# Kernel optimization log

Measured on AMD Instinct MI355X. Metric: run time of the kernel, lower is better.

## Reference

```python
import jax, jax.numpy as jnp
import numpy as np

TOKENS = 8192
IN_F = 4096
OUT_F = 4096
QMAX = 127.0  # int8 symmetric quant range
EPS = 1e-8


def setup_inputs() -> dict:
    key = jax.random.key(0)
    k1, k2, k3, k4 = jax.random.split(key, 4)
    x = jax.random.normal(k1, (TOKENS, IN_F), dtype=jnp.float32)
    # Pre-quantized int8 weight [out_features, in_features]
    weight_q = jax.random.randint(k2, (OUT_F, IN_F), -127, 128, dtype=jnp.int8)
    # Per-output-channel weight scales (realistic small magnitudes)
    weight_scale = jax.random.uniform(k3, (OUT_F,), dtype=jnp.float32) * 0.01 + 1e-3
    bias = jax.random.normal(k4, (OUT_F,), dtype=jnp.float32)
    return {"x": x, "weight_q": weight_q, "weight_scale": weight_scale, "bias": bias}


def reference(x, weight_q, weight_scale, bias):
    # Dynamic per-token symmetric int8 activation quantization
    absmax = jnp.max(jnp.abs(x), axis=-1, keepdims=True)           # [T, 1]
    x_scale = jnp.maximum(absmax, EPS) / QMAX                      # [T, 1]
    x_q = jnp.clip(jnp.round(x / x_scale), -QMAX, QMAX).astype(jnp.int8)
    acc = jax.lax.dot_general(
        x_q, weight_q,
        dimension_numbers=(((1,), (1,)), ((), ())),
        preferred_element_type=jnp.int32,
    )
    # Inline dequant: per-token activation scale * per-channel weight scale
    out = acc.astype(jnp.float32) * x_scale * weight_scale[None, :]
    out = out + bias[None, :]
    return out
```

## Files before the change

### kernel.cpp

```cpp
#include <hip/hip_runtime.h>
#include <cstdint>
#include <cstddef>

#define TOKENS 8192
#define IN_F   4096
#define OUT_F  4096
#define QMAXF  127.0f
#define EPSF   1e-8f

typedef int   int32x4 __attribute__((ext_vector_type(4)));

__device__ __forceinline__ void gload16(const void* g, void* l) {
    __builtin_amdgcn_global_load_lds(
        (const __attribute__((address_space(1))) void*)g,
        (__attribute__((address_space(3))) void*)l,
        16, 0, 0);
}

__device__ __forceinline__ int quant1(float v, float inv) {
    int q = (int)rintf(v * inv);
    q = q > 127 ? 127 : q;
    q = q < -127 ? -127 : q;
    return q;
}

__device__ __forceinline__ unsigned int pack4i(int a, int b, int c, int d) {
    return (unsigned int)(a & 255) | ((unsigned int)(b & 255) << 8) |
           ((unsigned int)(c & 255) << 16) | ((unsigned int)(d & 255) << 24);
}

__global__ __launch_bounds__(256) void quant_x_kernel(const float* __restrict__ x,
                                                      signed char* __restrict__ xq,
                                                      float* __restrict__ xscale) {
    const int t   = blockIdx.x;
    const int tid = threadIdx.x;
    const float* xr = x + (size_t)t * IN_F + tid * 16;

    float4 v[4];
    float am = 0.0f;
#pragma unroll
    for (int i = 0; i < 4; ++i) {
        v[i] = ((const float4*)xr)[i];
        am = fmaxf(am, fmaxf(fmaxf(fabsf(v[i].x), fabsf(v[i].y)),
                             fmaxf(fabsf(v[i].z), fabsf(v[i].w))));
    }
#pragma unroll
    for (int off = 32; off >= 1; off >>= 1)
        am = fmaxf(am, __shfl_xor(am, off));

    __shared__ float wmax[4];
    const int wid = tid >> 6, lane = tid & 63;
    if (lane == 0) wmax[wid] = am;
    __syncthreads();
    am = fmaxf(fmaxf(wmax[0], wmax[1]), fmaxf(wmax[2], wmax[3]));

    const float s   = fmaxf(am, EPSF) / QMAXF;
    const float inv = QMAXF / fmaxf(am, EPSF);
    if (tid == 0) xscale[t] = s;

    unsigned int w[4];
#pragma unroll
    for (int i = 0; i < 4; ++i) {
        w[i] = pack4i(quant1(v[i].x, inv), quant1(v[i].y, inv),
                      quant1(v[i].z, inv), quant1(v[i].w, inv));
    }
    *(uint4*)(xq + (size_t)t * IN_F + tid * 16) = make_uint4(w[0], w[1], w[2], w[3]);
}

__global__ __launch_bounds__(256) void pack_w_kernel(const int* __restrict__ w,
                                                     signed char* __restrict__ wq) {
    const size_t idx = (size_t)blockIdx.x * 256 + threadIdx.x;
    const int4* src = (const int4*)w + idx * 4;
    unsigned int o[4];
#pragma unroll
    for (int i = 0; i < 4; ++i) {
        int4 u = src[i];
        o[i] = pack4i(u.x, u.y, u.z, u.w);
    }
    ((uint4*)wq)[idx] = make_uint4(o[0], o[1], o[2], o[3]);
}

__global__ __launch_bounds__(256) void gemm_kernel(const signed char* __restrict__ xq,
                                                   const signed char* __restrict__ wq,
                                                   const float* __restrict__ xscale,
                                                   const float* __restrict__ wscale,
                                                   const float* __restrict__ bias,
                                                   float* __restrict__ out) {
    __shared__ __align__(16) signed char As[128 * 64];
    __shared__ __align__(16) signed char Bs[128 * 64];

    const int tid  = threadIdx.x;
    const int wid  = tid >> 6;
    const int lane = tid & 63;
    const int bid  = blockIdx.x;
    const int bn0  = (bid & 31) * 128;
    const int bm0  = (bid >> 5) * 128;

    const int rt = tid >> 2;
    const int ct = (tid & 3) * 16;
    const signed char* pa0 = xq + (size_t)(bm0 + rt) * IN_F + ct;
    const signed char* pa1 = xq + (size_t)(bm0 + 64 + rt) * IN_F + ct;
    const signed char* pb0 = wq + (size_t)(bn0 + rt) * IN_F + ct;
    const signed char* pb1 = wq + (size_t)(bn0 + 64 + rt) * IN_F + ct;
    signed char* lA0 = As + wid * 1024;
    signed char* lA1 = As + 4096 + wid * 1024;
    signed char* lB0 = Bs + wid * 1024;
    signed char* lB1 = Bs + 4096 + wid * 1024;

    const int wr = wid >> 1, wc = wid & 1;
    const int rA = wr * 64 + (lane & 15);
    const int rB = wc * 64 + (lane & 15);
    const int kb = (lane >> 4) * 16;

    int32x4 acc[4][4] = {};

    for (int kt = 0; kt < IN_F; kt += 64) {
        gload16(pa0 + kt, lA0);
        gload16(pa1 + kt, lA1);
        gload16(pb0 + kt, lB0);
        gload16(pb1 + kt, lB1);
        __syncthreads();

        int32x4 a[4], b[4];
#pragma unroll
        for (int m = 0; m < 4; ++m)
            a[m] = *(const int32x4*)&As[(rA + m * 16) * 64 + kb];
#pragma unroll
        for (int n = 0; n < 4; ++n)
            b[n] = *(const int32x4*)&Bs[(rB + n * 16) * 64 + kb];
#pragma unroll
        for (int m = 0; m < 4; ++m)
#pragma unroll
            for (int n = 0; n < 4; ++n)
                acc[m][n] = __builtin_amdgcn_mfma_i32_16x16x64_i8(a[m], b[n], acc[m][n], 0, 0, 0);
        __syncthreads();
    }

    const int r0 = bm0 + wr * 64 + (lane >> 4) * 4;
    const int c0 = bn0 + wc * 64 + (lane & 15);
#pragma unroll
    for (int n = 0; n < 4; ++n) {
        const int col = c0 + n * 16;
        const float wsc = wscale[col];
        const float bv  = bias[col];
#pragma unroll
        for (int m = 0; m < 4; ++m) {
#pragma unroll
            for (int j = 0; j < 4; ++j) {
                const int row = r0 + m * 16 + j;
                out[(size_t)row * OUT_F + col] =
                    (float)acc[m][n][j] * xscale[row] * wsc + bv;
            }
        }
    }
}

extern "C" void kernel_launch(void* const* d_in, const int* in_sizes, int n_in,
                              void* d_out, int out_size, void* d_ws, size_t ws_size,
                              hipStream_t stream) {
    const float* x      = (const float*)d_in[0];
    const int*   w      = (const int*)d_in[1];
    const float* wscale = (const float*)d_in[2];
    const float* bias   = (const float*)d_in[3];
    float* out = (float*)d_out;

    char* ws = (char*)d_ws;
    signed char* xq  = (signed char*)ws;
    signed char* wq8 = (signed char*)(ws + (size_t)TOKENS * IN_F);
    float* xscale    = (float*)(ws + (size_t)TOKENS * IN_F + (size_t)OUT_F * IN_F);

    quant_x_kernel<<<TOKENS, 256, 0, stream>>>(x, xq, xscale);
    pack_w_kernel<<<(OUT_F * (IN_F / 16)) / 256, 256, 0, stream>>>(w, wq8);
    gemm_kernel<<<(TOKENS / 128) * (OUT_F / 128), 256, 0, stream>>>(
        xq, wq8, xscale, wscale, bias, out);
}
```

Baseline: 235.0 us.

## Rewrite int8 GEMM with 256x256 tiles, triple-buffered LDS pipeline and 32x32 MFMA

```diff
diff --git a/kernel.cpp b/kernel.cpp
--- a/kernel.cpp
+++ b/kernel.cpp
@@ -8,13 +8,25 @@
 #define QMAXF  127.0f
 #define EPSF   1e-8f
 
-typedef int   int32x4 __attribute__((ext_vector_type(4)));
+typedef int i32x4  __attribute__((ext_vector_type(4)));
+typedef int i32x16 __attribute__((ext_vector_type(16)));
+
+#define BKB 64
+#define NT  (IN_F / BKB)
+#define LDS_BUF   32768
+#define LDS_TOTAL (3 * LDS_BUF)
 
 __device__ __forceinline__ void gload16(const void* g, void* l) {
     __builtin_amdgcn_global_load_lds(
         (const __attribute__((address_space(1))) void*)g,
         (__attribute__((address_space(3))) void*)l,
         16, 0, 0);
+}
+
+__device__ __forceinline__ void bar() {
+    asm volatile("" ::: "memory");
+    __builtin_amdgcn_s_barrier();
+    asm volatile("" ::: "memory");
 }
 
 __device__ __forceinline__ int quant1(float v, float inv) {
@@ -80,76 +92,143 @@
     ((uint4*)wq)[idx] = make_uint4(o[0], o[1], o[2], o[3]);
 }
 
-__global__ __launch_bounds__(256) void gemm_kernel(const signed char* __restrict__ xq,
-                                                   const signed char* __restrict__ wq,
-                                                   const float* __restrict__ xscale,
-                                                   const float* __restrict__ wscale,
-                                                   const float* __restrict__ bias,
-                                                   float* __restrict__ out) {
-    __shared__ __align__(16) signed char As[128 * 64];
-    __shared__ __align__(16) signed char Bs[128 * 64];
+__global__ __launch_bounds__(512, 2) void gemm_kernel(const signed char* __restrict__ xq,
+                                                      const signed char* __restrict__ wq,
+                                                      const float* __restrict__ xscale,
+                                                      const float* __restrict__ wscale,
+                                                      const float* __restrict__ bias,
+                                                      float* __restrict__ out) {
+    extern __shared__ __align__(16) char lds[];
 
     const int tid  = threadIdx.x;
     const int wid  = tid >> 6;
     const int lane = tid & 63;
+    const int wr   = wid >> 2;
+    const int wc   = wid & 3;
     const int bid  = blockIdx.x;
-    const int bn0  = (bid & 31) * 128;
-    const int bm0  = (bid >> 5) * 128;
-
-    const int rt = tid >> 2;
-    const int ct = (tid & 3) * 16;
-    const signed char* pa0 = xq + (size_t)(bm0 + rt) * IN_F + ct;
-    const signed char* pa1 = xq + (size_t)(bm0 + 64 + rt) * IN_F + ct;
-    const signed char* pb0 = wq + (size_t)(bn0 + rt) * IN_F + ct;
-    const signed char* pb1 = wq + (size_t)(bn0 + 64 + rt) * IN_F + ct;
-    signed char* lA0 = As + wid * 1024;
-    signed char* lA1 = As + 4096 + wid * 1024;
-    signed char* lB0 = Bs + wid * 1024;
-    signed char* lB1 = Bs + 4096 + wid * 1024;
-
-    const int wr = wid >> 1, wc = wid & 1;
-    const int rA = wr * 64 + (lane & 15);
-    const int rB = wc * 64 + (lane & 15);
-    const int kb = (lane >> 4) * 16;
-
-    int32x4 acc[4][4] = {};
-
-    for (int kt = 0; kt < IN_F; kt += 64) {
-        gload16(pa0 + kt, lA0);
-        gload16(pa1 + kt, lA1);
-        gload16(pb0 + kt, lB0);
-        gload16(pb1 + kt, lB1);
-        __syncthreads();
-
-        int32x4 a[4], b[4];
+    const int bm0  = (bid & 31) * 256;
+    const int bn0  = (bid >> 5) * 256;
+
+    const int srow = tid >> 2;
+    const int sg   = tid & 3;
+    const int scol = ((sg ^ (srow & 3)) << 4);
+    const signed char* gA0 = xq + (size_t)(bm0 + srow)       * IN_F + scol;
+    const signed char* gA1 = xq + (size_t)(bm0 + 128 + srow) * IN_F + scol;
+    const signed char* gB0 = wq + (size_t)(bn0 + srow)       * IN_F + scol;
+    const signed char* gB1 = wq + (size_t)(bn0 + 128 + srow) * IN_F + scol;
+    const int ldst = tid * 16;
+
+    const int l31 = lane & 31, hi = lane >> 5, l3 = lane & 3;
+    int a_off[4][2], b_off[2][2];
+#pragma unroll
+    for (int m = 0; m < 4; ++m) {
+        const int row = wr * 128 + m * 32 + l31;
+#pragma unroll
+        for (int ks = 0; ks < 2; ++ks)
+            a_off[m][ks] = row * 64 + (((ks * 2 + hi) ^ l3) << 4);
+    }
+#pragma unroll
+    for (int n = 0; n < 2; ++n) {
+        const int row = wc * 64 + n * 32 + l31;
+#pragma unroll
+        for (int ks = 0; ks < 2; ++ks)
+            b_off[n][ks] = 16384 + row * 64 + (((ks * 2 + hi) ^ l3) << 4);
+    }
+
+    i32x16 acc[4][2];
+#pragma unroll
+    for (int m = 0; m < 4; ++m)
+#pragma unroll
+        for (int n = 0; n < 2; ++n)
+#pragma unroll
+            for (int r = 0; r < 16; ++r) acc[m][n][r] = 0;
+
+    {
+        char* S0 = lds;
+        gload16(gA0,       S0 + ldst);
+        gload16(gA1,       S0 + 8192  + ldst);
+        gload16(gB0,       S0 + 16384 + ldst);
+        gload16(gB1,       S0 + 24576 + ldst);
+        char* S1 = lds + LDS_BUF;
+        gload16(gA0 + BKB, S1 + ldst);
+        gload16(gA1 + BKB, S1 + 8192  + ldst);
+        gload16(gB0 + BKB, S1 + 16384 + ldst);
+        gload16(gB1 + BKB, S1 + 24576 + ldst);
+    }
+    asm volatile("s_waitcnt vmcnt(4)" ::: "memory");
+    bar();
+
+    int cur = 0, nxt = 2;
+    for (int t = 0; t < NT; ++t) {
+        const char* Ab = lds + cur * LDS_BUF;
+        char* Sd = lds + nxt * LDS_BUF;
+        const bool st = (t + 2 < NT);
+        const int koff = (t + 2) * BKB;
+
+        i32x4 a0[4], b0[2];
+#pragma unroll
+        for (int m = 0; m < 4; ++m) a0[m] = *(const i32x4*)(Ab + a_off[m][0]);
+#pragma unroll
+        for (int n = 0; n < 2; ++n) b0[n] = *(const i32x4*)(Ab + b_off[n][0]);
+        if (st) {
+            gload16(gA0 + koff, Sd + ldst);
+            gload16(gB0 + koff, Sd + 16384 + ldst);
+        }
+        bar();
+        __builtin_amdgcn_s_setprio(1);
 #pragma unroll
         for (int m = 0; m < 4; ++m)
-            a[m] = *(const int32x4*)&As[(rA + m * 16) * 64 + kb];
-#pragma unroll
-        for (int n = 0; n < 4; ++n)
-            b[n] = *(const int32x4*)&Bs[(rB + n * 16) * 64 + kb];
+#pragma unroll
+            for (int n = 0; n < 2; ++n)
+                acc[m][n] = __builtin_amdgcn_mfma_i32_32x32x32_i8(a0[m], b0[n], acc[m][n], 0, 0, 0);
+        __builtin_amdgcn_s_setprio(0);
+        bar();
+
+        i32x4 a1[4], b1[2];
+#pragma unroll
+        for (int m = 0; m < 4; ++m) a1[m] = *(const i32x4*)(Ab + a_off[m][1]);
+#pragma unroll
+        for (int n = 0; n < 2; ++n) b1[n] = *(const i32x4*)(Ab + b_off[n][1]);
+        if (st) {
+            gload16(gA1 + koff, Sd + 8192  + ldst);
+            gload16(gB1 + koff, Sd + 24576 + ldst);
+        }
+        bar();
+        __builtin_amdgcn_s_setprio(1);
 #pragma unroll
         for (int m = 0; m < 4; ++m)
 #pragma unroll
-            for (int n = 0; n < 4; ++n)
-                acc[m][n] = __builtin_amdgcn_mfma_i32_16x16x64_i8(a[m], b[n], acc[m][n], 0, 0, 0);
-        __syncthreads();
-    }
-
-    const int r0 = bm0 + wr * 64 + (lane >> 4) * 4;
-    const int c0 = bn0 + wc * 64 + (lane & 15);
-#pragma unroll
-    for (int n = 0; n < 4; ++n) {
-        const int col = c0 + n * 16;
-        const float wsc = wscale[col];
-        const float bv  = bias[col];
-#pragma unroll
-        for (int m = 0; m < 4; ++m) {
-#pragma unroll
-            for (int j = 0; j < 4; ++j) {
-                const int row = r0 + m * 16 + j;
-                out[(size_t)row * OUT_F + col] =
-                    (float)acc[m][n][j] * xscale[row] * wsc + bv;
+            for (int n = 0; n < 2; ++n)
+                acc[m][n] = __builtin_amdgcn_mfma_i32_32x32x32_i8(a1[m], b1[n], acc[m][n], 0, 0, 0);
+        __builtin_amdgcn_s_setprio(0);
+
+        if (t + 2 < NT) {
+            asm volatile("s_waitcnt vmcnt(4)" ::: "memory");
+        } else if (t + 1 < NT) {
+            asm volatile("s_waitcnt vmcnt(0)" ::: "memory");
+        }
+        bar();
+
+        cur = (cur == 2) ? 0 : cur + 1;
+        nxt = (nxt == 2) ? 0 : nxt + 1;
+    }
+
+#pragma unroll
+    for (int m = 0; m < 4; ++m) {
+        const int rbase = bm0 + wr * 128 + m * 32 + 4 * hi;
+        float xsv[16];
+#pragma unroll
+        for (int r = 0; r < 16; ++r)
+            xsv[r] = xscale[rbase + (r & 3) + 8 * (r >> 2)];
+#pragma unroll
+        for (int n = 0; n < 2; ++n) {
+            const int col = bn0 + wc * 64 + n * 32 + l31;
+            const float wsc = wscale[col];
+            const float bv  = bias[col];
+#pragma unroll
+            for (int r = 0; r < 16; ++r) {
+                const int row = rbase + (r & 3) + 8 * (r >> 2);
+                out[(size_t)row * OUT_F + col] = (float)acc[m][n][r] * xsv[r] * wsc + bv;
             }
         }
     }
@@ -169,8 +248,11 @@
     signed char* wq8 = (signed char*)(ws + (size_t)TOKENS * IN_F);
     float* xscale    = (float*)(ws + (size_t)TOKENS * IN_F + (size_t)OUT_F * IN_F);
 
+    hipFuncSetAttribute((const void*)gemm_kernel,
+                        hipFuncAttributeMaxDynamicSharedMemorySize, LDS_TOTAL);
+
     quant_x_kernel<<<TOKENS, 256, 0, stream>>>(x, xq, xscale);
     pack_w_kernel<<<(OUT_F * (IN_F / 16)) / 256, 256, 0, stream>>>(w, wq8);
-    gemm_kernel<<<(TOKENS / 128) * (OUT_F / 128), 256, 0, stream>>>(
+    gemm_kernel<<<(TOKENS / 256) * (OUT_F / 256), 512, LDS_TOTAL, stream>>>(
         xq, wq8, xscale, wscale, bias, out);
 }
```

Measured after the change: 211.3 us. 10.1% less time.
